# Optimization experiments

Hardware: AMD Instinct MI355X
Metric: run time of the kernel (lower is better)

## Reference

```python
import jax, jax.numpy as jnp
import numpy as np
from jax import lax

N = 50000      # total nodes
E = 400000     # total edges
F = 512        # input feature dim
B = 50         # graphs in batch
NP = 1000      # nodes per graph
OUT = 10       # out_channel
EPS = 1e-5


def setup_inputs():
    key = jax.random.key(0)
    ks = jax.random.split(key, 20)
    x = jax.random.normal(ks[0], (N, F), jnp.float32)
    eg = jnp.arange(E) // (E // B)                       # graph id per edge
    src = jax.random.randint(ks[1], (E,), 0, NP) + eg * NP
    dst = jax.random.randint(ks[2], (E,), 0, NP) + eg * NP
    edge_index = jnp.stack([src, dst]).astype(jnp.int32)
    batch = (jnp.arange(N) // NP).astype(jnp.int32)
    s = 0.02
    W1 = s * jax.random.normal(ks[3], (1024, F), jnp.float32)
    b1 = jnp.zeros((1024,), jnp.float32)
    g1 = jnp.ones((1024,), jnp.float32)
    be1 = jnp.zeros((1024,), jnp.float32)
    Wp = s * jax.random.normal(ks[4], (1, 2 * 1024), jnp.float32)  # EdgePooling lin
    bp = jnp.zeros((1,), jnp.float32)
    W2 = s * jax.random.normal(ks[5], (512, 1024), jnp.float32)
    b2 = jnp.zeros((512,), jnp.float32)
    g2 = jnp.ones((512,), jnp.float32)
    be2 = jnp.zeros((512,), jnp.float32)
    Wfc = s * jax.random.normal(ks[6], (200, 512), jnp.float32)
    bfc = jnp.zeros((200,), jnp.float32)
    Wfc1 = s * jax.random.normal(ks[7], (OUT, 200), jnp.float32)
    bfc1 = jnp.zeros((OUT,), jnp.float32)
    return dict(x=x, edge_index=edge_index, batch=batch, W1=W1, b1=b1, g1=g1,
                be1=be1, Wp=Wp, bp=bp, W2=W2, b2=b2, g2=g2, be2=be2,
                Wfc=Wfc, bfc=bfc, Wfc1=Wfc1, bfc1=bfc1)


def _bn(h, g, b):
    m = h.mean(0)
    v = jnp.var(h, axis=0)  # biased var, as torch BatchNorm1d (train mode)
    return (h - m) * (g / jnp.sqrt(v + EPS)) + b


def _edge_pool(h, src, dst, batch, Wp, bp):
    # raw edge score: Linear([h_src || h_dst]) -> scalar per edge
    e = jnp.concatenate([h[src], h[dst]], axis=-1) @ Wp.T + bp  # [E,1]
    e = e[:, 0]
    # softmax over edges sharing the same destination node (PyG default)
    m = jax.ops.segment_max(e, dst, num_segments=N)
    ex = jnp.exp(e - m[dst])
    den = jax.ops.segment_sum(ex, dst, num_segments=N)
    score = ex / den[dst] + 0.5  # add_to_edge_score = 0.5

    # greedy contraction in descending-score order (sequential, like PyG)
    order = jnp.argsort(-score)
    so, do = src[order], dst[order]

    def step(merged, sd):
        s_, d_ = sd
        ok = (~merged[s_]) & (~merged[d_])
        merged = merged.at[s_].set(merged[s_] | ok)
        merged = merged.at[d_].set(merged[d_] | ok)
        return merged, ok

    _, valid = lax.scan(step, jnp.zeros(N, bool), (so, do))
    ec = (jnp.cumsum(valid.astype(jnp.int32)) - 1)      # cluster id per contracted edge
    num_merged = valid.astype(jnp.int32).sum()

    OOB = jnp.int32(N)
    cluster = jnp.full((N,), -1, jnp.int32)
    cluster = cluster.at[jnp.where(valid, so, OOB)].set(ec, mode='drop')
    cluster = cluster.at[jnp.where(valid, do, OOB)].set(ec, mode='drop')
    unmerged = cluster < 0
    rank = jnp.cumsum(unmerged.astype(jnp.int32)) - 1
    cluster = jnp.where(unmerged, num_merged + rank, cluster)

    # per-cluster multiplier: contracted-edge score, 1.0 for singleton nodes
    mult = jnp.ones((N,), h.dtype)
    mult = mult.at[jnp.where(valid, ec, OOB)].set(score[order], mode='drop')

    new_x = jax.ops.segment_sum(h, cluster, num_segments=N) * mult[:, None]
    new_batch = jnp.full((N,), B, jnp.int32).at[cluster].set(batch)  # pad slots -> dummy graph B
    return new_x, new_batch


def reference(x, edge_index, batch, W1, b1, g1, be1, Wp, bp, W2, b2, g2, be2,
              Wfc, bfc, Wfc1, bfc1):
    src, dst = edge_index[0], edge_index[1]
    # ChebConv K=1 == plain linear (only T_0 = x term)
    h = jax.nn.relu(_bn(x @ W1.T + b1, g1, be1))         # [N,1024]
    h, nb = _edge_pool(h, src, dst, batch, Wp, bp)       # [N,1024] padded, [N]
    h = jax.nn.relu(_bn(h @ W2.T + b2, g2, be2))         # [N,512]
    # global mean pool over graphs (dummy segment B holds padding)
    sums = jax.ops.segment_sum(h, nb, num_segments=B + 1)[:B]
    cnt = jax.ops.segment_sum(jnp.ones((N,), h.dtype), nb, num_segments=B + 1)[:B]
    pooled = sums / jnp.maximum(cnt, 1.0)[:, None]       # [B,512]
    hid = jax.nn.relu(pooled @ Wfc.T + bfc)              # [B,200]; dropout is eval no-op
    return hid @ Wfc1.T + bfc1                           # [B,OUT]
```

## Files before the change

### kernel.cpp

```cpp
#include <hip/hip_runtime.h>

#define Nn   50000
#define Ee   400000
#define Ff   512
#define H1   1024
#define H2   512
#define Bb   50
#define OUTd 10
#define EPSc 1e-5f
#define NPg  1000
#define EPg  8000

typedef _Float16 h8 __attribute__((ext_vector_type(8)));
typedef _Float16 h4 __attribute__((ext_vector_type(4)));
typedef float f4 __attribute__((ext_vector_type(4)));

__device__ __forceinline__ unsigned fmap(float f) {
    unsigned u = __float_as_uint(f);
    return (u & 0x80000000u) ? ~u : (u | 0x80000000u);
}
__device__ __forceinline__ float funmap(unsigned m) {
    unsigned u = (m & 0x80000000u) ? (m ^ 0x80000000u) : ~m;
    return __uint_as_float(u);
}

__device__ __forceinline__ void gl_lds16(const void* g, void* l) {
    __builtin_amdgcn_global_load_lds(
        (const __attribute__((address_space(1))) unsigned int*)g,
        (__attribute__((address_space(3))) unsigned int*)l,
        16, 0, 0);
}

__global__ void prep_kernel(const float* __restrict__ x, _Float16* __restrict__ xhi, _Float16* __restrict__ xlo,
                            const float* __restrict__ W1, _Float16* __restrict__ w1h, _Float16* __restrict__ w1l,
                            const float* __restrict__ W2, _Float16* __restrict__ w2h,
                            double* __restrict__ cs1, double* __restrict__ css1,
                            double* __restrict__ cs2, double* __restrict__ css2, int* __restrict__ scal) {
    int i = blockIdx.x * blockDim.x + threadIdx.x;
    int nth = gridDim.x * blockDim.x;
    for (int j = i; j < H1; j += nth) { cs1[j] = 0.0; css1[j] = 0.0; }
    for (int j = i; j < H2; j += nth) { cs2[j] = 0.0; css2[j] = 0.0; }
    if (i < 16) scal[i] = 0;
    const int nx = Nn * Ff / 4, nw1 = H1 * Ff / 4, nw2 = H2 * H1 / 4;
    for (int k = i; k < nx; k += nth) {
        float4 v = ((const float4*)x)[k];
        h4 H = { (_Float16)v.x, (_Float16)v.y, (_Float16)v.z, (_Float16)v.w };
        h4 L = { (_Float16)(v.x - (float)H[0]), (_Float16)(v.y - (float)H[1]),
                 (_Float16)(v.z - (float)H[2]), (_Float16)(v.w - (float)H[3]) };
        ((h4*)xhi)[k] = H;
        ((h4*)xlo)[k] = L;
    }
    for (int k = i; k < nw1; k += nth) {
        float4 v = ((const float4*)W1)[k];
        h4 H = { (_Float16)v.x, (_Float16)v.y, (_Float16)v.z, (_Float16)v.w };
        h4 L = { (_Float16)(v.x - (float)H[0]), (_Float16)(v.y - (float)H[1]),
                 (_Float16)(v.z - (float)H[2]), (_Float16)(v.w - (float)H[3]) };
        ((h4*)w1h)[k] = H;
        ((h4*)w1l)[k] = L;
    }
    for (int k = i; k < nw2; k += nth) {
        float4 v = ((const float4*)W2)[k];
        h4 H = { (_Float16)v.x, (_Float16)v.y, (_Float16)v.z, (_Float16)v.w };
        ((h4*)w2h)[k] = H;
    }
}

__global__ __launch_bounds__(512) void gemm1_256_kernel(
        const _Float16* __restrict__ Ahi, const _Float16* __restrict__ Alo,
        const _Float16* __restrict__ Bhi, const _Float16* __restrict__ Blo,
        const float* __restrict__ bias, float* __restrict__ C,
        double* __restrict__ csum, double* __restrict__ cssum)
{
    const int M = Nn;
    const int nwg = gridDim.x, orig = blockIdx.x;
    const int qq = nwg >> 3, rr = nwg & 7;
    const int xcd = orig & 7, idx = orig >> 3;
    const int lin = (xcd < rr ? xcd * (qq + 1) : rr * (qq + 1) + (xcd - rr) * qq) + idx;
    const int nT = H1 / 256;
    const int bmI = lin / nT;
    const int bm = bmI * 256, bn = (lin - bmI * nT) * 256;
    __shared__ __align__(16) _Float16 smem[2][4][256 * 32];
    const int tid = threadIdx.x, lane = tid & 63, wave = tid >> 6;
    const int rIn = lane >> 2;
    const int kSrcByte = ((((lane & 3) - ((lane >> 3) & 3)) & 3) << 4);
    const int wr = wave >> 2, wc = wave & 3;
    const int lr = lane & 15, kb = lane >> 4;
    const int pGr = ((kb + ((lr >> 1) & 3)) & 3) << 3;
    const int arr = wave >> 1;
    const int hv = wave & 1;
    const bool isA = (arr < 2);
    const _Float16* gp = (arr == 0) ? Ahi : (arr == 1) ? Alo : (arr == 2) ? Bhi : Blo;
    const int tb = isA ? bm : bn;
    f4 acc[8][4] = {};

    auto STAGE = [&](int b, int k0) {
        _Float16* lp = smem[b][arr] + hv * (128 * 32);
#pragma unroll
        for (int c = 0; c < 8; ++c) {
            int row = tb + hv * 128 + c * 16 + rIn;
            if (isA) row = min(row, M - 1);
            gl_lds16((const char*)gp + ((size_t)row * Ff + k0) * 2 + kSrcByte, lp + c * 512);
        }
    };

    int cur = 0;
    STAGE(0, 0);
    for (int k0 = 0; k0 < Ff; k0 += 32) {
        __syncthreads();
        if (k0 + 32 < Ff) STAGE(cur ^ 1, k0 + 32);
        const _Float16* AhP = smem[cur][0];
        const _Float16* AlP = smem[cur][1];
        const _Float16* BhP = smem[cur][2];
        const _Float16* BlP = smem[cur][3];
        h8 ahf[8], alf[8];
#pragma unroll
        for (int mi = 0; mi < 8; ++mi) {
            const int ar = (wr * 128 + mi * 16 + lr) * 32 + pGr;
            ahf[mi] = *(const h8*)&AhP[ar];
            alf[mi] = *(const h8*)&AlP[ar];
        }
#pragma unroll
        for (int ni = 0; ni < 4; ++ni) {
            const int br = (wc * 64 + ni * 16 + lr) * 32 + pGr;
            const h8 bh = *(const h8*)&BhP[br];
            const h8 bl = *(const h8*)&BlP[br];
#pragma unroll
            for (int mi = 0; mi < 8; ++mi) {
                acc[mi][ni] = __builtin_amdgcn_mfma_f32_16x16x32_f16(ahf[mi], bh, acc[mi][ni], 0, 0, 0);
                acc[mi][ni] = __builtin_amdgcn_mfma_f32_16x16x32_f16(ahf[mi], bl, acc[mi][ni], 0, 0, 0);
                acc[mi][ni] = __builtin_amdgcn_mfma_f32_16x16x32_f16(alf[mi], bh, acc[mi][ni], 0, 0, 0);
            }
        }
        cur ^= 1;
    }
#pragma unroll
    for (int ni = 0; ni < 4; ++ni) {
        const int col = bn + wc * 64 + ni * 16 + lr;
        const float bv = bias[col];
        double sd_ = 0.0, ssd = 0.0;
#pragma unroll
        for (int mi = 0; mi < 8; ++mi)
#pragma unroll
            for (int r = 0; r < 4; ++r) {
                int row = bm + wr * 128 + mi * 16 + kb * 4 + r;
                if (row < M) {
                    float v = acc[mi][ni][r] + bv;
                    C[(size_t)row * H1 + col] = v;
                    sd_ += (double)v;
                    ssd += (double)v * (double)v;
                }
            }
        sd_ += __shfl_xor(sd_, 16); ssd += __shfl_xor(ssd, 16);
        sd_ += __shfl_xor(sd_, 32); ssd += __shfl_xor(ssd, 32);
        if (kb == 0) {
            atomicAdd(&csum[col], sd_);
            atomicAdd(&cssum[col], ssd);
        }
    }
}

__global__ __launch_bounds__(256) void gemm2_kernel(
        const _Float16* __restrict__ Ag, const _Float16* __restrict__ Bh,
        const float* __restrict__ bias, float* __restrict__ C,
        const int* __restrict__ Mptr, int nT,
        double* __restrict__ csum, double* __restrict__ cssum)
{
    const int M = Mptr[0];
    const int nwg = gridDim.x, orig = blockIdx.x;
    const int qq = nwg >> 3, rr = nwg & 7;
    const int xcd = orig & 7, idx = orig >> 3;
    const int lin = (xcd < rr ? xcd * (qq + 1) : rr * (qq + 1) + (xcd - rr) * qq) + idx;
    const int bmI = lin / nT;
    const int bm = bmI * 128, bn = (lin - bmI * nT) * 128;
    if (bm >= M) return;
    __shared__ __align__(16) _Float16 smem[2][2][128 * 32];
    const int tid = threadIdx.x, lane = tid & 63, wave = tid >> 6;
    const int rIn = lane >> 2;
    const int kSrcByte = ((((lane & 3) - ((lane >> 3) & 3)) & 3) << 4);
    const int wr = wave >> 1, wc = wave & 1;
    const int lr = lane & 15, kb = lane >> 4;
    const int pGr = ((kb + ((lr >> 1) & 3)) & 3) << 3;
    f4 acc[4][4] = {};

    auto STAGE = [&](int b, int k0) {
        const bool isA = (wave < 2);
        const _Float16* gp = isA ? Ag : Bh;
        _Float16* lp = smem[b][isA ? 0 : 1];
        const int tb = isA ? bm : bn;
        const int hf = wave & 1;
#pragma unroll
        for (int c2 = 0; c2 < 4; ++c2) {
            int c = hf * 4 + c2;
            int row = tb + c * 16 + rIn;
            if (isA) row = min(row, M - 1);
            gl_lds16((const char*)gp + ((size_t)row * H1 + k0) * 2 + kSrcByte, lp + c * 512);
        }
    };

    int cur = 0;
    STAGE(0, 0);
    for (int k0 = 0; k0 < H1; k0 += 32) {
        __syncthreads();
        if (k0 + 32 < H1) STAGE(cur ^ 1, k0 + 32);
        const _Float16* AhP = smem[cur][0];
        const _Float16* BhP = smem[cur][1];
        const int ar = (wr * 64 + lr) * 32 + pGr;
        const int br = (wc * 64 + lr) * 32 + pGr;
        h8 ahf[4], bhf[4];
#pragma unroll
        for (int i = 0; i < 4; ++i) {
            ahf[i] = *(const h8*)&AhP[ar + i * 512];
            bhf[i] = *(const h8*)&BhP[br + i * 512];
        }
#pragma unroll
        for (int mi = 0; mi < 4; ++mi)
#pragma unroll
            for (int ni = 0; ni < 4; ++ni)
                acc[mi][ni] = __builtin_amdgcn_mfma_f32_16x16x32_f16(ahf[mi], bhf[ni], acc[mi][ni], 0, 0, 0);
        cur ^= 1;
    }
#pragma unroll
    for (int ni = 0; ni < 4; ++ni) {
        const int col = bn + wc * 64 + ni * 16 + lr;
        const float bv = bias[col];
        double sd_ = 0.0, ssd = 0.0;
#pragma unroll
        for (int mi = 0; mi < 4; ++mi)
#pragma unroll
            for (int r = 0; r < 4; ++r) {
                int row = bm + wr * 64 + mi * 16 + kb * 4 + r;
                if (row < M) {
                    float v = acc[mi][ni][r] + bv;
                    C[(size_t)row * H2 + col] = v;
                    sd_ += (double)v;
                    ssd += (double)v * (double)v;
                }
            }
        sd_ += __shfl_xor(sd_, 16); ssd += __shfl_xor(ssd, 16);
        sd_ += __shfl_xor(sd_, 32); ssd += __shfl_xor(ssd, 32);
        if (kb == 0) {
            atomicAdd(&csum[col], sd_);
            atomicAdd(&cssum[col], ssd);
        }
    }
}

__global__ void bnparam_kernel(const double* __restrict__ s, const double* __restrict__ ss,
                               const float* __restrict__ g, const float* __restrict__ be,
                               float* __restrict__ a, float* __restrict__ bb, int cols,
                               const float* __restrict__ padBias, const int* __restrict__ CvPtr) {
    int j = blockIdx.x * blockDim.x + threadIdx.x;
    if (j >= cols) return;
    double sum = s[j], sumsq = ss[j];
    if (CvPtr) {
        double pad = (double)(Nn - CvPtr[0]);
        double bv = padBias ? (double)padBias[j] : 0.0;
        sum += pad * bv; sumsq += pad * bv * bv;
    }
    double mean = sum / (double)Nn;
    double var = sumsq / (double)Nn - mean * mean;
    float aj = g[j] / sqrtf((float)var + EPSc);
    a[j] = aj;
    bb[j] = be[j] - (float)mean * aj;
}

__global__ __launch_bounds__(256) void pq_kernel(const float* __restrict__ h,
        const float* __restrict__ a, const float* __restrict__ bb,
        const float* __restrict__ Wp, float* __restrict__ p, float* __restrict__ q) {
    const int n = blockIdx.x * 4 + (threadIdx.x >> 6);
    if (n >= Nn) return;
    const int lane = threadIdx.x & 63;
    float sp = 0.f, sq = 0.f;
    const float* row = h + (size_t)n * H1;
#pragma unroll
    for (int u = 0; u < 4; ++u) {
        int j = u * 256 + lane * 4;
        float4 v = *(const float4*)(row + j);
        const float4 av = *(const float4*)(a + j);
        const float4 bv = *(const float4*)(bb + j);
        v.x = fmaxf(v.x * av.x + bv.x, 0.f);
        v.y = fmaxf(v.y * av.y + bv.y, 0.f);
        v.z = fmaxf(v.z * av.z + bv.z, 0.f);
        v.w = fmaxf(v.w * av.w + bv.w, 0.f);
        const float4 wp = *(const float4*)(Wp + j);
        const float4 wq = *(const float4*)(Wp + H1 + j);
        sp += v.x * wp.x + v.y * wp.y + v.z * wp.z + v.w * wp.w;
        sq += v.x * wq.x + v.y * wq.y + v.z * wq.z + v.w * wq.w;
    }
#pragma unroll
    for (int off = 32; off > 0; off >>= 1) {
        sp += __shfl_xor(sp, off);
        sq += __shfl_xor(sq, off);
    }
    if (lane == 0) { p[n] = sp; q[n] = sq; }
}

__global__ __launch_bounds__(1024) void match_fused_kernel(
        const int* __restrict__ ei,
        const float* __restrict__ p, const float* __restrict__ q,
        const float* __restrict__ bp,
        unsigned long long* __restrict__ packed,
        int* __restrict__ nodeA, int* __restrict__ nodeB,
        float* __restrict__ multc, int* __restrict__ scal,
        int* __restrict__ gbase, int* __restrict__ gcnt) {
    __shared__ __align__(16) char LB[52096];
    unsigned short* lst = (unsigned short*)LB;
    float* earr = (float*)LB;
    float* pl = (float*)(LB + 32000);
    float* ql = pl + NPg;
    unsigned long long* best = (unsigned long long*)(LB + 32000);
    unsigned* maxu = (unsigned*)(LB + 40000);
    int* mergedS = (int*)(LB + 40000);
    unsigned long long* den = (unsigned long long*)(LB + 44000);
    float* lmult = (float*)(LB + 44000);
    unsigned short* lsA = (unsigned short*)(LB + 48000);
    unsigned short* ldA = (unsigned short*)(LB + 50000);
    int* cnts = (int*)(LB + 52032);

    const int g = blockIdx.x;
    const int tid = threadIdx.x;
    const int e0 = g * EPg, n0 = g * NPg;
    const int* srcp = ei + e0;
    const int* dstp = ei + Ee + e0;
    const float bpv = bp[0];

    for (int i = tid; i < NPg; i += 1024) {
        pl[i] = p[n0 + i];
        ql[i] = q[n0 + i];
        maxu[i] = 0u;
        den[i] = 0ull;
    }
    __syncthreads();
    for (int i = tid; i < EPg; i += 1024) {
        int s = srcp[i] - n0, d = dstp[i] - n0;
        float e = pl[s] + ql[d] + bpv;
        earr[i] = e;
        atomicMax(&maxu[d], fmap(e));
    }
    __syncthreads();
    for (int i = tid; i < EPg; i += 1024) {
        int d = dstp[i] - n0;
        float ex = expf(earr[i] - funmap(maxu[d]));
        atomicAdd(&den[d], (unsigned long long)(ex * 4294967296.0f));
    }
    __syncthreads();
    for (int i = tid; i < EPg; i += 1024) {
        int s = srcp[i] - n0, d = dstp[i] - n0;
        float ex = expf(earr[i] - funmap(maxu[d]));
        float den_f = (float)((double)den[d] * (1.0 / 4294967296.0));
        float sc = ex / den_f + 0.5f;
        packed[e0 + i] = ((unsigned long long)__float_as_uint(sc) << 33)
                       | ((unsigned long long)(8191u - (unsigned)i) << 20)
                       | ((unsigned long long)(unsigned)s << 10) | (unsigned long long)(unsigned)d;
    }
    __syncthreads();
    for (int i = tid; i < NPg; i += 1024) mergedS[i] = 0;
    for (int i = tid; i < EPg; i += 1024) lst[i] = (unsigned short)i;
    if (tid == 0) { cnts[0] = EPg; cnts[1] = 0; cnts[2] = 0; }
    __syncthreads();
    int cur = 0;
    for (int round = 0; round < 20000; ++round) {
        const int n_cur = cnts[cur];
        if (n_cur == 0) break;
        if (tid == 0) cnts[cur ^ 1] = 0;
        for (int i = tid; i < NPg; i += 1024) best[i] = 0ull;
        __syncthreads();
        for (int ii = tid; ii < n_cur; ii += 1024) {
            int le = lst[cur * EPg + ii];
            unsigned long long pk = packed[e0 + le];
            int s = (int)((pk >> 10) & 1023), d = (int)(pk & 1023);
            if (mergedS[s] | mergedS[d]) { lst[cur * EPg + ii] = 0xFFFF; continue; }
            atomicMax(&best[s], pk);
            atomicMax(&best[d], pk);
        }
        __syncthreads();
        for (int ii = tid; ii < n_cur; ii += 1024) {
            int le = lst[cur * EPg + ii];
            if (le == 0xFFFF) continue;
            unsigned long long pk = packed[e0 + le];
            int s = (int)((pk >> 10) & 1023), d = (int)(pk & 1023);
            if (best[s] == pk && best[d] == pk) {
                int c = atomicAdd(&cnts[2], 1);
                lsA[c] = (unsigned short)s;
                ldA[c] = (s == d) ? (unsigned short)0xFFFF : (unsigned short)d;
                lmult[c] = __uint_as_float((unsigned)(pk >> 33));
                mergedS[s] = 1;
                if (d != s) mergedS[d] = 1;
            } else {
                int pos = atomicAdd(&cnts[cur ^ 1], 1);
                lst[(cur ^ 1) * EPg + pos] = (unsigned short)le;
            }
        }
        __syncthreads();
        cur ^= 1;
    }
    for (int i = tid; i < NPg; i += 1024) {
        if (!mergedS[i]) {
            int c = atomicAdd(&cnts[2], 1);
            lsA[c] = (unsigned short)i;
            ldA[c] = 0xFFFF;
            lmult[c] = 1.0f;
        }
    }
    __syncthreads();
    if (tid == 0) {
        int ncl = cnts[2];
        int base = atomicAdd(&scal[2], ncl);
        cnts[3] = base;
        gbase[g] = base;
        gcnt[g] = ncl;
    }
    __syncthreads();
    const int ncl = cnts[2], base = cnts[3];
    for (int i = tid; i < ncl; i += 1024) {
        nodeA[base + i] = n0 + (int)lsA[i];
        nodeB[base + i] = (ldA[i] == 0xFFFF) ? -1 : (n0 + (int)ldA[i]);
        multc[base + i] = lmult[i];
    }
}

__global__ __launch_bounds__(256) void gather_kernel(const float* __restrict__ h,
        const float* __restrict__ a, const float* __restrict__ bb,
        const int* __restrict__ nodeA, const int* __restrict__ nodeB,
        const float* __restrict__ multc, const int* __restrict__ scal,
        _Float16* __restrict__ Ag) {
    int c = blockIdx.x * 4 + (threadIdx.x >> 6);
    if (c >= scal[2]) return;
    const int lane = threadIdx.x & 63;
    int na = nodeA[c], nb = nodeB[c];
    float mu = multc[c];
#pragma unroll
    for (int u = 0; u < 4; ++u) {
        int j = u * 256 + lane * 4;
        const float4 av = *(const float4*)(a + j);
        const float4 bv = *(const float4*)(bb + j);
        float4 v = *(const float4*)(h + (size_t)na * H1 + j);
        v.x = fmaxf(v.x * av.x + bv.x, 0.f);
        v.y = fmaxf(v.y * av.y + bv.y, 0.f);
        v.z = fmaxf(v.z * av.z + bv.z, 0.f);
        v.w = fmaxf(v.w * av.w + bv.w, 0.f);
        if (nb >= 0) {
            float4 w = *(const float4*)(h + (size_t)nb * H1 + j);
            v.x += fmaxf(w.x * av.x + bv.x, 0.f);
            v.y += fmaxf(w.y * av.y + bv.y, 0.f);
            v.z += fmaxf(w.z * av.z + bv.z, 0.f);
            v.w += fmaxf(w.w * av.w + bv.w, 0.f);
        }
        h4 o = { (_Float16)(mu * v.x), (_Float16)(mu * v.y), (_Float16)(mu * v.z), (_Float16)(mu * v.w) };
        *(h4*)(Ag + (size_t)c * H1 + j) = o;
    }
}

__global__ __launch_bounds__(256) void pool_seg_kernel(const float* __restrict__ C2,
        const float* __restrict__ a2, const float* __restrict__ bb2,
        const int* __restrict__ gbase, const int* __restrict__ gcnt,
        float* __restrict__ pool) {
    const int g = blockIdx.x;
    const int j = blockIdx.y * 256 + threadIdx.x;
    const int b0 = gbase[g], cN = gcnt[g];
    const float aj = a2[j], bj = bb2[j];
    float s = 0.f;
    for (int c = b0; c < b0 + cN; ++c)
        s += fmaxf(C2[(size_t)c * H2 + j] * aj + bj, 0.f);
    pool[g * H2 + j] = s;
}

__global__ void fc1_kernel(const float* __restrict__ pool, const int* __restrict__ gcnt,
                           const float* __restrict__ Wfc, const float* __restrict__ bfc,
                           float* __restrict__ hid) {
    int g = blockIdx.x;
    int o = threadIdx.x;
    float inv = 1.0f / fmaxf((float)gcnt[g], 1.0f);
    if (o < 200) {
        float s = 0.f;
        for (int j = 0; j < H2; ++j) s += (pool[g * H2 + j] * inv) * Wfc[o * H2 + j];
        hid[g * 200 + o] = fmaxf(s + bfc[o], 0.f);
    }
}
__global__ void fc2_kernel(const float* __restrict__ hid, const float* __restrict__ Wfc1,
                           const float* __restrict__ bfc1, float* __restrict__ out) {
    int idx = threadIdx.x;
    if (idx < Bb * OUTd) {
        int g = idx / OUTd, o = idx % OUTd;
        float s = bfc1[o];
        for (int t = 0; t < 200; ++t) s += hid[g * 200 + t] * Wfc1[o * 200 + t];
        out[idx] = s;
    }
}

extern "C" void kernel_launch(void* const* d_in, const int* in_sizes, int n_in,
                              void* d_out, int out_size, void* d_ws, size_t ws_size,
                              hipStream_t stream) {
    (void)in_sizes; (void)n_in; (void)out_size; (void)ws_size;
    const float* x    = (const float*)d_in[0];
    const int*   ei   = (const int*)d_in[1];
    const float* W1   = (const float*)d_in[3];
    const float* b1   = (const float*)d_in[4];
    const float* g1   = (const float*)d_in[5];
    const float* be1  = (const float*)d_in[6];
    const float* Wp   = (const float*)d_in[7];
    const float* bp   = (const float*)d_in[8];
    const float* W2   = (const float*)d_in[9];
    const float* b2   = (const float*)d_in[10];
    const float* g2   = (const float*)d_in[11];
    const float* be2  = (const float*)d_in[12];
    const float* Wfc  = (const float*)d_in[13];
    const float* bfc  = (const float*)d_in[14];
    const float* Wfc1 = (const float*)d_in[15];
    const float* bfc1 = (const float*)d_in[16];

    char* w = (char*)d_ws;
    auto take = [&](size_t bytes) -> char* {
        char* r = w;
        w += (bytes + 255) & ~(size_t)255;
        return r;
    };
    float* h      = (float*)take((size_t)Nn * H1 * 4);
    _Float16* xhi = (_Float16*)take((size_t)Nn * Ff * 2);
    _Float16* xlo = (_Float16*)take((size_t)Nn * Ff * 2);
    _Float16* w1h = (_Float16*)take((size_t)H1 * Ff * 2);
    _Float16* w1l = (_Float16*)take((size_t)H1 * Ff * 2);
    _Float16* w2h = (_Float16*)take((size_t)H2 * H1 * 2);
    float* p      = (float*)take((size_t)Nn * 4);
    float* q      = (float*)take((size_t)Nn * 4);
    unsigned long long* packed = (unsigned long long*)take((size_t)Ee * 8);
    int* nodeA    = (int*)take((size_t)Nn * 4);
    int* nodeB    = (int*)take((size_t)Nn * 4);
    float* multc  = (float*)take((size_t)Nn * 4);
    double* cs1   = (double*)take((size_t)H1 * 8);
    double* css1  = (double*)take((size_t)H1 * 8);
    double* cs2   = (double*)take((size_t)H2 * 8);
    double* css2  = (double*)take((size_t)H2 * 8);
    float* a1     = (float*)take((size_t)H1 * 4);
    float* bb1    = (float*)take((size_t)H1 * 4);
    float* a2     = (float*)take((size_t)H2 * 4);
    float* bb2    = (float*)take((size_t)H2 * 4);
    float* pool   = (float*)take((size_t)Bb * H2 * 4);
    float* hid    = (float*)take((size_t)Bb * 200 * 4);
    int* scal     = (int*)take(64 * 4);
    int* gbase    = (int*)take(64 * 4);
    int* gcnt     = (int*)take(64 * 4);
    _Float16* Ag  = xhi;
    float* C2o    = h;

    const int mT  = (Nn + 127) / 128;
    const int mT2 = (Nn + 255) / 256;

    prep_kernel<<<dim3(2048), dim3(256), 0, stream>>>(x, xhi, xlo, W1, w1h, w1l, W2, w2h,
                                                      cs1, css1, cs2, css2, scal);
    gemm1_256_kernel<<<dim3(mT2 * (H1 / 256)), dim3(512), 0, stream>>>(
        xhi, xlo, w1h, w1l, b1, h, cs1, css1);
    bnparam_kernel<<<dim3((H1 + 255) / 256), dim3(256), 0, stream>>>(cs1, css1, g1, be1, a1, bb1, H1, (const float*)nullptr, (const int*)nullptr);
    pq_kernel<<<dim3((Nn + 3) / 4), dim3(256), 0, stream>>>(h, a1, bb1, Wp, p, q);
    match_fused_kernel<<<dim3(Bb), dim3(1024), 0, stream>>>(ei, p, q, bp, packed,
        nodeA, nodeB, multc, scal, gbase, gcnt);
    gather_kernel<<<dim3((Nn + 3) / 4), dim3(256), 0, stream>>>(h, a1, bb1, nodeA, nodeB, multc, scal, Ag);
    gemm2_kernel<<<dim3(mT * (H2 / 128)), dim3(256), 0, stream>>>(
        Ag, w2h, b2, C2o, scal + 2, H2 / 128, cs2, css2);
    bnparam_kernel<<<dim3((H2 + 255) / 256), dim3(256), 0, stream>>>(cs2, css2, g2, be2, a2, bb2, H2, b2, scal + 2);
    pool_seg_kernel<<<dim3(Bb, H2 / 256), dim3(256), 0, stream>>>(C2o, a2, bb2, gbase, gcnt, pool);
    fc1_kernel<<<dim3(Bb), dim3(256), 0, stream>>>(pool, gcnt, Wfc, bfc, hid);
    fc2_kernel<<<dim3(1), dim3(512), 0, stream>>>(hid, Wfc1, bfc1, (float*)d_out);
}
```

Baseline: 666.8 us.

## Shrink GEMM1 tiles to 128x128 with single-buffered LDS staging

Replaces the 256x256-tile, 512-thread double-buffered first GEMM with a 128x128-tile, 256-thread kernel that loads each k-slice into one shared buffer and synchronizes before and after compute. This cuts shared-memory use per block, which may allow more resident blocks per CU and smaller tail effects. In exchange it gives up overlap of global loads with MFMA work and lowers operand reuse per tile, increasing global/LDS traffic.

```diff
diff --git a/kernel.cpp b/kernel.cpp
--- a/kernel.cpp
+++ b/kernel.cpp
@@ -65,7 +65,7 @@
     }
 }
 
-__global__ __launch_bounds__(512) void gemm1_256_kernel(
+__global__ __launch_bounds__(256) void gemm1_mfma_kernel(
         const _Float16* __restrict__ Ahi, const _Float16* __restrict__ Alo,
         const _Float16* __restrict__ Bhi, const _Float16* __restrict__ Blo,
         const float* __restrict__ bias, float* __restrict__ C,
@@ -76,62 +76,57 @@
     const int qq = nwg >> 3, rr = nwg & 7;
     const int xcd = orig & 7, idx = orig >> 3;
     const int lin = (xcd < rr ? xcd * (qq + 1) : rr * (qq + 1) + (xcd - rr) * qq) + idx;
-    const int nT = H1 / 256;
+    const int nT = H1 / 128;
     const int bmI = lin / nT;
-    const int bm = bmI * 256, bn = (lin - bmI * nT) * 256;
-    __shared__ __align__(16) _Float16 smem[2][4][256 * 32];
+    const int bm = bmI * 128, bn = (lin - bmI * nT) * 128;
+    if (bm >= M) return;
+    __shared__ __align__(16) _Float16 smem[4][128 * 32];
     const int tid = threadIdx.x, lane = tid & 63, wave = tid >> 6;
     const int rIn = lane >> 2;
     const int kSrcByte = ((((lane & 3) - ((lane >> 3) & 3)) & 3) << 4);
-    const int wr = wave >> 2, wc = wave & 3;
+    const int wr = wave >> 1, wc = wave & 1;
     const int lr = lane & 15, kb = lane >> 4;
     const int pGr = ((kb + ((lr >> 1) & 3)) & 3) << 3;
-    const int arr = wave >> 1;
-    const int hv = wave & 1;
-    const bool isA = (arr < 2);
-    const _Float16* gp = (arr == 0) ? Ahi : (arr == 1) ? Alo : (arr == 2) ? Bhi : Blo;
+    f4 acc[4][4] = {};
+
+    const _Float16* gp = (wave == 0) ? Ahi : (wave == 1) ? Alo : (wave == 2) ? Bhi : Blo;
+    const bool isA = (wave < 2);
     const int tb = isA ? bm : bn;
-    f4 acc[8][4] = {};
-
-    auto STAGE = [&](int b, int k0) {
-        _Float16* lp = smem[b][arr] + hv * (128 * 32);
-#pragma unroll
-        for (int c = 0; c < 8; ++c) {
-            int row = tb + hv * 128 + c * 16 + rIn;
-            if (isA) row = min(row, M - 1);
-            gl_lds16((const char*)gp + ((size_t)row * Ff + k0) * 2 + kSrcByte, lp + c * 512);
-        }
-    };
-
-    int cur = 0;
-    STAGE(0, 0);
+
     for (int k0 = 0; k0 < Ff; k0 += 32) {
+        {
+            _Float16* lp = smem[wave];
+#pragma unroll
+            for (int c = 0; c < 8; ++c) {
+                int row = tb + c * 16 + rIn;
+                if (isA) row = min(row, M - 1);
+                gl_lds16((const char*)gp + ((size_t)row * Ff + k0) * 2 + kSrcByte, lp + c * 512);
+            }
+        }
         __syncthreads();
-        if (k0 + 32 < Ff) STAGE(cur ^ 1, k0 + 32);
-        const _Float16* AhP = smem[cur][0];
-        const _Float16* AlP = smem[cur][1];
-        const _Float16* BhP = smem[cur][2];
-        const _Float16* BlP = smem[cur][3];
-        h8 ahf[8], alf[8];
-#pragma unroll
-        for (int mi = 0; mi < 8; ++mi) {
-            const int ar = (wr * 128 + mi * 16 + lr) * 32 + pGr;
-            ahf[mi] = *(const h8*)&AhP[ar];
-            alf[mi] = *(const h8*)&AlP[ar];
-        }
-#pragma unroll
-        for (int ni = 0; ni < 4; ++ni) {
-            const int br = (wc * 64 + ni * 16 + lr) * 32 + pGr;
-            const h8 bh = *(const h8*)&BhP[br];
-            const h8 bl = *(const h8*)&BlP[br];
-#pragma unroll
-            for (int mi = 0; mi < 8; ++mi) {
-                acc[mi][ni] = __builtin_amdgcn_mfma_f32_16x16x32_f16(ahf[mi], bh, acc[mi][ni], 0, 0, 0);
-                acc[mi][ni] = __builtin_amdgcn_mfma_f32_16x16x32_f16(ahf[mi], bl, acc[mi][ni], 0, 0, 0);
-                acc[mi][ni] = __builtin_amdgcn_mfma_f32_16x16x32_f16(alf[mi], bh, acc[mi][ni], 0, 0, 0);
+        const _Float16* AhP = smem[0];
+        const _Float16* AlP = smem[1];
+        const _Float16* BhP = smem[2];
+        const _Float16* BlP = smem[3];
+        const int ar = (wr * 64 + lr) * 32 + pGr;
+        const int br = (wc * 64 + lr) * 32 + pGr;
+        h8 ahf[4], bhf[4], alf[4], blf[4];
+#pragma unroll
+        for (int i = 0; i < 4; ++i) {
+            ahf[i] = *(const h8*)&AhP[ar + i * 512];
+            bhf[i] = *(const h8*)&BhP[br + i * 512];
+            alf[i] = *(const h8*)&AlP[ar + i * 512];
+            blf[i] = *(const h8*)&BlP[br + i * 512];
+        }
+#pragma unroll
+        for (int mi = 0; mi < 4; ++mi)
+#pragma unroll
+            for (int ni = 0; ni < 4; ++ni) {
+                acc[mi][ni] = __builtin_amdgcn_mfma_f32_16x16x32_f16(ahf[mi], bhf[ni], acc[mi][ni], 0, 0, 0);
+                acc[mi][ni] = __builtin_amdgcn_mfma_f32_16x16x32_f16(ahf[mi], blf[ni], acc[mi][ni], 0, 0, 0);
+                acc[mi][ni] = __builtin_amdgcn_mfma_f32_16x16x32_f16(alf[mi], bhf[ni], acc[mi][ni], 0, 0, 0);
             }
-        }
-        cur ^= 1;
+        __syncthreads();
     }
 #pragma unroll
     for (int ni = 0; ni < 4; ++ni) {
@@ -139,10 +134,10 @@
         const float bv = bias[col];
         double sd_ = 0.0, ssd = 0.0;
 #pragma unroll
-        for (int mi = 0; mi < 8; ++mi)
+        for (int mi = 0; mi < 4; ++mi)
 #pragma unroll
             for (int r = 0; r < 4; ++r) {
-                int row = bm + wr * 128 + mi * 16 + kb * 4 + r;
+                int row = bm + wr * 64 + mi * 16 + kb * 4 + r;
                 if (row < M) {
                     float v = acc[mi][ni][r] + bv;
                     C[(size_t)row * H1 + col] = v;
@@ -544,11 +539,10 @@
     float* C2o    = h;
 
     const int mT  = (Nn + 127) / 128;
-    const int mT2 = (Nn + 255) / 256;
 
     prep_kernel<<<dim3(2048), dim3(256), 0, stream>>>(x, xhi, xlo, W1, w1h, w1l, W2, w2h,
                                                       cs1, css1, cs2, css2, scal);
-    gemm1_256_kernel<<<dim3(mT2 * (H1 / 256)), dim3(512), 0, stream>>>(
+    gemm1_mfma_kernel<<<dim3(mT * (H1 / 128)), dim3(256), 0, stream>>>(
         xhi, xlo, w1h, w1l, b1, h, cs1, css1);
     bnparam_kernel<<<dim3((H1 + 255) / 256), dim3(256), 0, stream>>>(cs1, css1, g1, be1, a1, bb1, H1, (const float*)nullptr, (const int*)nullptr);
     pq_kernel<<<dim3((Nn + 3) / 4), dim3(256), 0, stream>>>(h, a1, bb1, Wp, p, q);
```

Result: slower. 701.7 us (+5.2%).
